# Kernel tuning notes

Hardware: AMD Instinct MI355X
Metric: run time of the kernel (lower is better)

Reference implementation:

```python
import jax, jax.numpy as jnp
import numpy as np

B, L, DIM = 8, 512, 8          # batch, seq len, raw channels (value dim D = 2*DIM = 16)
ET, HID, H = 128, 128, 2       # embed_time, hidden_size, num_heads
MAXLEN = 512
NEG = -1e9


def setup_inputs() -> dict:
    key = jax.random.key(0)
    ks = jax.random.split(key, 40)
    def n(i, shape, s=0.05):
        return jax.random.normal(ks[i], shape, jnp.float32) * s
    vals = jax.random.normal(ks[0], (B, L, DIM), jnp.float32)
    msk = (jax.random.uniform(ks[1], (B, L, DIM)) > 0.2).astype(jnp.float32)
    x = jnp.concatenate([vals, msk], -1)                      # (B, L, 2*DIM)
    time_steps = jax.random.uniform(ks[2], (B, L), jnp.float32)
    return {
        'x': x, 'time_steps': time_steps,
        # learned time embedding: Linear(1, ET-1) periodic + Linear(1,1)
        'w_per': n(3, (1, ET - 1)), 'b_per': n(4, (ET - 1,)),
        'w_lin': n(5, (1, 1)), 'b_lin': n(6, (1,)),
        # MultiTimeAttention projections
        'Wq_t': n(7, (ET, ET)), 'bq_t': n(8, (ET,)),
        'Wk_t': n(9, (ET, ET)), 'bk_t': n(10, (ET,)),
        'Wo_t': n(11, (2 * DIM * H, HID)), 'bo_t': n(12, (HID,)),
        'pos_emb': n(13, (MAXLEN + 1, HID)), 'cls_emb': n(14, (1, HID)),
        # transformer block (BERT-style post-LN encoder layer, d_ff=HID)
        'tWq': n(15, (HID, HID)), 'tbq': n(16, (HID,)),
        'tWk': n(17, (HID, HID)), 'tbk': n(18, (HID,)),
        'tWv': n(19, (HID, HID)), 'tbv': n(20, (HID,)),
        'tWo': n(21, (HID, HID)), 'tbo': n(22, (HID,)),
        'ln1_g': jnp.ones((HID,), jnp.float32), 'ln1_b': jnp.zeros((HID,), jnp.float32),
        'fW1': n(23, (HID, HID)), 'fb1': n(24, (HID,)),
        'fW2': n(25, (HID, HID)), 'fb2': n(26, (HID,)),
        'ln2_g': jnp.ones((HID,), jnp.float32), 'ln2_b': jnp.zeros((HID,), jnp.float32),
        # BertPooler
        'pW': n(27, (HID, HID)), 'pb': n(28, (HID,)),
    }


def _time_emb(tt, w_per, b_per, w_lin, b_lin):
    tt = tt[..., None]                                        # (B, L, 1)
    return jnp.concatenate([tt @ w_lin + b_lin, jnp.sin(tt @ w_per + b_per)], -1)


def _ln(x, g, b, eps=1e-5):
    m = x.mean(-1, keepdims=True)
    v = ((x - m) ** 2).mean(-1, keepdims=True)
    return (x - m) / jnp.sqrt(v + eps) * g + b


def _mta(q_emb, k_emb, value, mask, Wq, bq, Wk, bk, Wo, bo):
    # MultiTimeAttention: scores broadcast to value-channel axis, softmax over keys
    D = value.shape[-1]
    dk = ET // H
    def split(e, W, b):
        p = e @ W + b
        return p.reshape(e.shape[0], -1, H, dk).transpose(0, 2, 1, 3)
    q = split(q_emb, Wq, bq)                                  # (Bq, H, Lq, dk)
    k = split(k_emb, Wk, bk)                                  # (B,  H, Lk, dk)
    scores = jnp.matmul(q, k.swapaxes(-1, -2)) / jnp.sqrt(jnp.float32(dk))  # (B,H,Lq,Lk)
    s5 = jnp.where(mask[:, None, None, :, :] == 0, NEG, scores[..., None])  # (B,H,Lq,Lk,D)
    p = jax.nn.softmax(s5, axis=-2)
    out = jnp.einsum('bhqkd,bkd->bhqd', p, value)             # (B, H, Lq, D)
    Bv = value.shape[0]
    out = out.transpose(0, 2, 1, 3).reshape(Bv, -1, H * D)
    return out @ Wo + bo


def _tblock(x, tWq, tbq, tWk, tbk, tWv, tbv, tWo, tbo, ln1_g, ln1_b,
            fW1, fb1, fW2, fb2, ln2_g, ln2_b):
    Bq, Lq, _ = x.shape
    dk = HID // H
    def heads(W, b):
        return (x @ W + b).reshape(Bq, Lq, H, dk).transpose(0, 2, 1, 3)
    q, k, v = heads(tWq, tbq), heads(tWk, tbk), heads(tWv, tbv)
    a = jax.nn.softmax(jnp.matmul(q, k.swapaxes(-1, -2)) / jnp.sqrt(jnp.float32(dk)), -1)
    o = jnp.matmul(a, v).transpose(0, 2, 1, 3).reshape(Bq, Lq, HID) @ tWo + tbo
    x = _ln(x + o, ln1_g, ln1_b)
    f = jax.nn.relu(x @ fW1 + fb1) @ fW2 + fb2
    return _ln(x + f, ln2_g, ln2_b)


def reference(x, time_steps, w_per, b_per, w_lin, b_lin,
              Wq_t, bq_t, Wk_t, bk_t, Wo_t, bo_t, pos_emb, cls_emb,
              tWq, tbq, tWk, tbk, tWv, tbv, tWo, tbo, ln1_g, ln1_b,
              fW1, fb1, fW2, fb2, ln2_g, ln2_b, pW, pb):
    Bx = x.shape[0]
    mask_half = x[:, :, DIM:]
    mask = jnp.concatenate([mask_half, mask_half], -1)        # (B, L, 2*DIM)
    key_e = _time_emb(time_steps, w_per, b_per, w_lin, b_lin)
    tq_e = _time_emb(time_steps, w_per, b_per, w_lin, b_lin)  # query_time_steps=None -> same
    cls_t = jnp.linspace(0.0, 1.0, 128, dtype=jnp.float32)[None]
    cls_q_e = _time_emb(cls_t, w_per, b_per, w_lin, b_lin)    # (1, 128, ET)
    cls_out = _mta(cls_q_e, key_e, x, mask, Wq_t, bq_t, Wk_t, bk_t, Wo_t, bo_t)
    out = _mta(tq_e, key_e, x, mask, Wq_t, bq_t, Wk_t, bk_t, Wo_t, bo_t)
    tb = (tWq, tbq, tWk, tbk, tWv, tbv, tWo, tbo, ln1_g, ln1_b,
          fW1, fb1, fW2, fb2, ln2_g, ln2_b)
    cls_repr = jnp.broadcast_to(cls_emb[None, :, :], (Bx, 1, HID))
    # encode(cls_out, is_pooling=True), pooling='bert': no pos emb, take token 0
    h = _tblock(jnp.concatenate([cls_repr, cls_out], 1), *tb)
    cls_pooling = jnp.tanh(h[:, 0] @ pW + pb)                 # (B, HID)
    # encode(out, is_pooling=False) [pretrain path]: pos emb + transformer, drop CLS
    h2 = jnp.concatenate([cls_repr, out], 1)                  # (B, L+1, HID)
    h2 = h2 + pos_emb[:h2.shape[1]][None]
    h2 = _tblock(h2, *tb)
    last_hidden_state = h2[:, 1:]                             # (B, L, HID)
    return cls_pooling, last_hidden_state
```

## Files before the change

### kernel.cpp

```cpp
#include <hip/hip_runtime.h>
#include <hip/hip_bf16.h>
#include <math.h>


static constexpr int NM_ = 8 * 513;
static constexpr int NC_ = 8 * 129;
static constexpr int NT_ = NM_ + NC_;
static constexpr int VTS_ = 5248;

using bf = __hip_bfloat16;
typedef __attribute__((ext_vector_type(8))) short bf16x8;
typedef __attribute__((ext_vector_type(4))) short bf16x4;
typedef __attribute__((ext_vector_type(4))) float floatx4;
typedef __attribute__((ext_vector_type(8))) unsigned short ushortx8;

__device__ __forceinline__ float wave_reduce_sum(float v) {
    #pragma unroll
    for (int off = 32; off >= 1; off >>= 1) v += __shfl_xor(v, off);
    return v;
}
__device__ __forceinline__ float wave_reduce_max(float v) {
    #pragma unroll
    for (int off = 32; off >= 1; off >>= 1) v = fmaxf(v, __shfl_xor(v, off));
    return v;
// ... 76 lines not shown
        if (idx < 128 * 14) {
            int n = idx / 14, c8 = idx - n * 14;
            ushortx8 z = {0, 0, 0, 0, 0, 0, 0, 0};
            *(ushortx8*)(a.vt + (size_t)n * VTS_ + 5136 + c8 * 8) = z;
        }
    }
}

struct GemmM {
    const void* A[3]; const unsigned short* W[3]; const float* bias[3];
    unsigned short* C[3];
    int M[3]; float bscale[3];
};
__global__ void __launch_bounds__(256)
gemm_mfma_kernel(GemmM p) {
    int y = blockIdx.y;
    const unsigned short* Wsw = p.W[y];
    const float* bias = p.bias[y];
    unsigned short* C = p.C[y];
    int M = p.M[y];
    float bscale = p.bscale[y];
    int m0 = blockIdx.x * 16;
    if (m0 >= M) return;
    int tid = threadIdx.x;
    int wv = tid >> 6, lane = tid & 63;
    int am = lane & 15, aq = lane >> 4;
    const unsigned short* A = (const unsigned short*)p.A[y];
    const unsigned short* Arow = A + (size_t)(m0 + am) * 128;
    floatx4 acc0 = {0.f, 0.f, 0.f, 0.f}, acc1 = acc0;
    #pragma unroll
    for (int ks = 0; ks < 4; ++ks) {
        bf16x8 af = *(const bf16x8*)(Arow + ks * 32 + aq * 8);
        const unsigned short* base = Wsw + ((size_t)ks * 8 + 2 * wv) * 512 + lane * 8;
        bf16x8 b0 = *(const bf16x8*)(base);
        bf16x8 b1 = *(const bf16x8*)(base + 512);
        acc0 = __builtin_amdgcn_mfma_f32_16x16x32_bf16(af, b0, acc0, 0, 0, 0);
        acc1 = __builtin_amdgcn_mfma_f32_16x16x32_bf16(af, b1, acc1, 0, 0, 0);
    }
    int col = lane & 15, rowb = (lane >> 4) * 4;
    #pragma unroll
    for (int t = 0; t < 2; ++t) {
        floatx4 acc = t ? acc1 : acc0;
        int n = wv * 32 + t * 16 + col;
        float bv = bias[n] * bscale;
        #pragma unroll
        for (int rg = 0; rg < 4; ++rg)
            C[(size_t)(m0 + rowb + rg) * 128 + n] = f2u(acc[rg] + bv);
    }
}

struct MaAtt { unsigned short sp[2][16][520]; float red[2][1280]; };
union MaU { MaAtt att; unsigned short qAs[16][136]; };

__global__ void __launch_bounds__(256, 2)
mta_fused_kernel(const unsigned short* qp_cls, const unsigned short* qp_main,
                 const unsigned short* kp, const unsigned short* btg,
                 const float* Wo, const float* bo, const float* cls_emb, const float* pos,
                 float* xin,
                 const unsigned short* Wq, const unsigned short* Wk, const unsigned short* Wv,
                 const float* bq, const float* bk, const float* bv_,
                 unsigned short* outq, unsigned short* outk, unsigned short* vT) {
    __shared__ MaU U;
    __shared__ float As32[16][36];
    int vb = blockIdx.x, tid = threadIdx.x;
    int lane = tid & 63, wv = tid >> 6;
    int m = lane & 15, g = lane >> 4;
    bool special = (vb == 320);
    int is_cls = 0, qt = 0, b = 0;
    if (!special) {
        if (vb < 256) { b = vb >> 5; qt = vb & 31; }
        else { int t = vb - 256; b = t >> 3; qt = t & 7; is_cls = 1; }
    }
    int q0 = qt * 16;

    if (!special) {
        const unsigned short* qrow = is_cls
            ? (qp_cls + (size_t)(q0 + m) * 128)
            : (qp_main + (size_t)(b * 512 + q0 + m) * 128);
        bf16x8 qf[2][2];
        #pragma unroll
        for (int h = 0; h < 2; ++h) {
            qf[h][0] = *(const bf16x8*)(qrow + h * 64 + g * 8);
            qf[h][1] = *(const bf16x8*)(qrow + h * 64 + 32 + g * 8);
        }
        const unsigned short* kbase = kp + ((size_t)b * 512) * 128;
        #pragma unroll
        for (int kt = 0; kt < 8; ++kt) {
            int colk = kt * 64 + wv * 16 + m;
            const unsigned short* kb = kbase + (size_t)colk * 128;
            #pragma unroll
            for (int h = 0; h < 2; ++h) {
                bf16x8 b0 = *(const bf16x8*)(kb + h * 64 + g * 8);
                bf16x8 b1 = *(const bf16x8*)(kb + h * 64 + 32 + g * 8);
                floatx4 acc = {0.f, 0.f, 0.f, 0.f};
                acc = __builtin_amdgcn_mfma_f32_16x16x32_bf16(qf[h][0], b0, acc, 0, 0, 0);
                acc = __builtin_amdgcn_mfma_f32_16x16x32_bf16(qf[h][1], b1, acc, 0, 0, 0);
                #pragma unroll
                for (int rg = 0; rg < 4; ++rg)
                    U.att.sp[h][g * 4 + rg][colk] = f2u(acc[rg]);
            }
        }
        __syncthreads();

        for (int rr2 = wv; rr2 < 32; rr2 += 4) {
            int h = rr2 >> 4, rr = rr2 & 15;
            float mx = -1e30f;
            #pragma unroll
            for (int k = 0; k < 8; ++k) mx = fmaxf(mx, u2f(U.att.sp[h][rr][k * 64 + lane]));
            mx = wave_reduce_max(mx);
            #pragma unroll
            for (int k = 0; k < 8; ++k)
                U.att.sp[h][rr][k * 64 + lane] = f2u(expf(u2f(U.att.sp[h][rr][k * 64 + lane]) - mx));
        }
        __syncthreads();

        floatx4 macc[2] = {{0.f,0.f,0.f,0.f},{0.f,0.f,0.f,0.f}};
        {
            const unsigned short* bbase = btg + ((size_t)(b * 16 + m)) * 512 + g * 8;
            #pragma unroll
            for (int cc = 0; cc < 4; ++cc) {
                int koff = (wv + cc * 4) * 32;
                bf16x8 bfv = *(const bf16x8*)(bbase + koff);
                #pragma unroll
                for (int h = 0; h < 2; ++h) {
                    bf16x8 af = *(const bf16x8*)&U.att.sp[h][m][koff + g * 8];
                    macc[h] = __builtin_amdgcn_mfma_f32_16x16x32_bf16(af, bfv, macc[h], 0, 0, 0);
                }
            }
        }
        #pragma unroll
        for (int h = 0; h < 2; ++h)
            #pragma unroll
            for (int rg = 0; rg < 4; ++rg)
                U.att.red[h][tid * 4 + rg] = macc[h][rg];
        __syncthreads();
        {
            int l = tid >> 2, rg = tid & 3;
            int row = (l >> 4) * 4 + rg, c = l & 15;
            #pragma unroll
            for (int h = 0; h < 2; ++h) {
                const float* rc = U.att.red[h];
                float s = rc[l * 4 + rg] + rc[(64 + l) * 4 + rg]
                        + rc[(128 + l) * 4 + rg] + rc[(192 + l) * 4 + rg];
                U.att.red[h][1024 + row * 16 + c] = s;
            }
        }
        __syncthreads();
        if (tid < 128) {
            int r = tid >> 3, c = tid & 7;
            #pragma unroll
            for (int h = 0; h < 2; ++h) {
                float num = U.att.red[h][1024 + r * 16 + c];
                float den = U.att.red[h][1024 + r * 16 + 8 + c];
                As32[r][h * 16 + c] = num / den;
                As32[r][h * 16 + 8 + c] = 1.0f;
            }
        }
        __syncthreads();
    }

    int r = tid >> 4, gi = tid & 15, c0 = gi * 8;
    int segbase = is_cls ? (NM_ + b * 129) : (b * 513);
    auto Rof = [&](int rr) -> int {
        if (special) return (rr < 8) ? rr * 513 : NM_ + (rr - 8) * 129;
        return segbase + 1 + q0 + rr;
    };
    int R = Rof(r);
    int prow;
    if (special) prow = (r < 8) ? 0 : -1;
    else prow = is_cls ? -1 : (1 + q0 + r);

    float acc[8];
    if (special) {
        #pragma unroll
        for (int j = 0; j < 8; ++j) acc[j] = cls_emb[c0 + j];
    } else {
        #pragma unroll
        for (int j = 0; j < 8; ++j) acc[j] = bo[c0 + j];
        #pragma unroll 8
        for (int k = 0; k < 32; ++k) {
            float a = As32[r][k];
            const float4 w0 = *(const float4*)(Wo + (size_t)k * 128 + c0);
            const float4 w1 = *(const float4*)(Wo + (size_t)k * 128 + c0 + 4);
            acc[0] = fmaf(a, w0.x, acc[0]); acc[1] = fmaf(a, w0.y, acc[1]);
            acc[2] = fmaf(a, w0.z, acc[2]); acc[3] = fmaf(a, w0.w, acc[3]);
            acc[4] = fmaf(a, w1.x, acc[4]); acc[5] = fmaf(a, w1.y, acc[5]);
            acc[6] = fmaf(a, w1.z, acc[6]); acc[7] = fmaf(a, w1.w, acc[7]);
        }
    }
    if (prow >= 0) {
        const float* pr = pos + (size_t)prow * 128 + c0;
        float4 p0 = *(const float4*)(pr);
        float4 p1 = *(const float4*)(pr + 4);
        acc[0] += p0.x; acc[1] += p0.y; acc[2] += p0.z; acc[3] += p0.w;
        acc[4] += p1.x; acc[5] += p1.y; acc[6] += p1.z; acc[7] += p1.w;
    }
    __syncthreads();
    *(float4*)(xin + (size_t)R * 128 + c0) = make_float4(acc[0], acc[1], acc[2], acc[3]);
    *(float4*)(xin + (size_t)R * 128 + c0 + 4) = make_float4(acc[4], acc[5], acc[6], acc[7]);
    *(ushort4*)&U.qAs[r][c0] = make_ushort4(f2u(acc[0]), f2u(acc[1]), f2u(acc[2]), f2u(acc[3]));
    *(ushort4*)&U.qAs[r][c0 + 4] = make_ushort4(f2u(acc[4]), f2u(acc[5]), f2u(acc[6]), f2u(acc[7]));
    __syncthreads();

    int am = lane & 15, aq = lane >> 4;
    int col = lane & 15, rowb = (lane >> 4) * 4;
    const unsigned short* Ws[3] = {Wq, Wk, Wv};
    const float* bs[3] = {bq, bk, bv_};
    float bsc[3] = {0.125f, 1.f, 1.f};
    unsigned short* Cs[2] = {outq, outk};
    #pragma unroll
    for (int y = 0; y < 3; ++y) {
        floatx4 acc0 = {0.f, 0.f, 0.f, 0.f}, acc1 = acc0;
        #pragma unroll
        for (int ks = 0; ks < 4; ++ks) {
            bf16x8 af = *(bf16x8*)&U.qAs[am][ks * 32 + aq * 8];
            const unsigned short* base = Ws[y] + ((size_t)ks * 8 + 2 * wv) * 512 + lane * 8;
            bf16x8 b0 = *(const bf16x8*)(base);
            bf16x8 b1 = *(const bf16x8*)(base + 512);
            acc0 = __builtin_amdgcn_mfma_f32_16x16x32_bf16(af, b0, acc0, 0, 0, 0);
            acc1 = __builtin_amdgcn_mfma_f32_16x16x32_bf16(af, b1, acc1, 0, 0, 0);
        }
        #pragma unroll
        for (int t = 0; t < 2; ++t) {
            floatx4 a2 = t ? acc1 : acc0;
            int n = wv * 32 + t * 16 + col;
            float bvv = bs[y][n] * bsc[y];
            #pragma unroll
            for (int rg = 0; rg < 4; ++rg) {
                unsigned short val = f2u(a2[rg] + bvv);
                int R2 = Rof(rowb + rg);
                if (y < 2) Cs[y][(size_t)R2 * 128 + n] = val;
                else       vT[(size_t)n * VTS_ + R2] = val;
            }
        }
    }
}

union TbU {
    unsigned short sp[2][16][588];
    struct { float Xs[16][128]; unsigned short Hs[16][136]; } ffn;
};

template<int NKT>
__device__ __forceinline__ void tb_attn_phase(
    const unsigned short* qp, const unsigned short* kp, const unsigned short* vT,
    int Lq, int base, int q0, int tid,
    unsigned short (&sp)[2][16][588], float (&rinv)[2][16],
    unsigned short (&As)[16][136])
{
    int lane = tid & 63, wv = tid >> 6;
    int m = lane & 15, g = lane >> 4;

    int qr = q0 + m; if (qr >= Lq) qr = Lq - 1;
    const unsigned short* qrow = qp + (size_t)(base + qr) * 128;
    bf16x8 qf[2][2];
    #pragma unroll
    for (int h = 0; h < 2; ++h) {
        qf[h][0] = *(const bf16x8*)(qrow + h * 64 + g * 8);
        qf[h][1] = *(const bf16x8*)(qrow + h * 64 + 32 + g * 8);
    }

    #pragma unroll
    for (int kt = 0; kt < NKT; ++kt) {
        int colk = kt * 64 + wv * 16 + m;
        int krow = (colk < Lq) ? colk : (Lq - 1);
        const unsigned short* kb = kp + (size_t)(base + krow) * 128;
        #pragma unroll
        for (int h = 0; h < 2; ++h) {
            bf16x8 b0 = *(const bf16x8*)(kb + h * 64 + g * 8);
            bf16x8 b1 = *(const bf16x8*)(kb + h * 64 + 32 + g * 8);
            floatx4 acc = {0.f, 0.f, 0.f, 0.f};
            acc = __builtin_amdgcn_mfma_f32_16x16x32_bf16(qf[h][0], b0, acc, 0, 0, 0);
            acc = __builtin_amdgcn_mfma_f32_16x16x32_bf16(qf[h][1], b1, acc, 0, 0, 0);
            #pragma unroll
            for (int rg = 0; rg < 4; ++rg)
                sp[h][g * 4 + rg][colk] = f2u((colk < Lq) ? acc[rg] : -1e30f);
        }
    }
    __syncthreads();

    for (int rr2 = wv; rr2 < 32; rr2 += 4) {
        int h = rr2 >> 4, rr = rr2 & 15;
        float mx = -1e30f;
        #pragma unroll
        for (int k = 0; k < NKT; ++k) mx = fmaxf(mx, u2f(sp[h][rr][k * 64 + lane]));
        mx = wave_reduce_max(mx);
        float sum = 0.f;
        #pragma unroll
        for (int k = 0; k < NKT; ++k) {
            float e = expf(u2f(sp[h][rr][k * 64 + lane]) - mx);
            sp[h][rr][k * 64 + lane] = f2u(e);
            sum += e;
        }
        sum = wave_reduce_sum(sum);
        if (lane == 0) rinv[h][rr] = 1.f / sum;
    }
    __syncthreads();

    floatx4 oacc[2] = {{0.f,0.f,0.f,0.f},{0.f,0.f,0.f,0.f}};
    #pragma unroll
    for (int kt = 0; kt < NKT; ++kt) {
        int k0 = kt * 64;
        #pragma unroll
        for (int h = 0; h < 2; ++h) {
            const unsigned short* vbase = vT + (size_t)(h * 64 + wv * 16 + m) * VTS_ + base;
            #pragma unroll
            for (int c = 0; c < 2; ++c) {
                bf16x4 plo = *(const bf16x4*)&sp[h][m][k0 + c * 32 + g * 8];
                bf16x4 phi = *(const bf16x4*)&sp[h][m][k0 + c * 32 + g * 8 + 4];
                bf16x8 vf = *(const bf16x8*)(vbase + k0 + c * 32 + g * 8);
                oacc[h] = __builtin_amdgcn_mfma_f32_16x16x32_bf16(join8(plo, phi), vf, oacc[h], 0, 0, 0);
            }
        }
    }
    int dcol = wv * 16 + m;
    #pragma unroll
    for (int h = 0; h < 2; ++h)
        #pragma unroll
        for (int rg = 0; rg < 4; ++rg) {
            int q = g * 4 + rg;
            As[q][h * 64 + dcol] = f2u(oacc[h][rg] * rinv[h][q]);
        }
    __syncthreads();
}

__global__ void __launch_bounds__(256, 2)
tb_fused_kernel(const unsigned short* qp, const unsigned short* kp,
                const unsigned short* vT, const float* resid,
                const unsigned short* Wao, const float* bao,
                const float* g1, const float* b1ln,
                const unsigned short* W1, const float* fb1,
                const unsigned short* W2, const float* fb2,
                const float* g2, const float* b2ln,
                const float* pW, const float* pb, float* dout) {
    __shared__ TbU U;
    __shared__ unsigned short As[16][136];
    __shared__ float rinv[2][16];
    __shared__ float redS[4][4][4], redQ[4][4][4], smean[16], sinv[16], x2row[128];
    __shared__ int poolb;

    int xx = blockIdx.x, b = blockIdx.y, tid = threadIdx.x;
    int is_cls = (xx >= 33);
    int qt = is_cls ? xx - 33 : xx;
    int Lq = is_cls ? 129 : 513;
    int base = is_cls ? (NM_ + b * 129) : (b * 513);
    int lane = tid & 63, wv = tid >> 6;
    int q0 = qt * 16, g = lane >> 4;
    if (tid == 0) poolb = -1;

    if (is_cls) tb_attn_phase<3>(qp, kp, vT, Lq, base, q0, tid, U.sp, rinv, As);
    else        tb_attn_phase<9>(qp, kp, vT, Lq, base, q0, tid, U.sp, rinv, As);

    int am = lane & 15, aq = lane >> 4;
    int col = lane & 15, rowb = g * 4;

    float ov[2][4];
    {
        floatx4 acc0 = {0.f, 0.f, 0.f, 0.f}, acc1 = acc0;
        #pragma unroll
        for (int ks = 0; ks < 4; ++ks) {
            bf16x8 af = *(bf16x8*)&As[am][ks * 32 + aq * 8];
            const unsigned short* wb = Wao + ((size_t)ks * 8 + 2 * wv) * 512 + lane * 8;
            bf16x8 bb0 = *(const bf16x8*)(wb);
            bf16x8 bb1 = *(const bf16x8*)(wb + 512);
            acc0 = __builtin_amdgcn_mfma_f32_16x16x32_bf16(af, bb0, acc0, 0, 0, 0);
            acc1 = __builtin_amdgcn_mfma_f32_16x16x32_bf16(af, bb1, acc1, 0, 0, 0);
        }
        #pragma unroll
        for (int t = 0; t < 2; ++t) {
            int n = wv * 32 + t * 16 + col;
            float bv = bao[n];
            floatx4 acc = t ? acc1 : acc0;
            #pragma unroll
            for (int rg = 0; rg < 4; ++rg) {
                int qo = q0 + rowb + rg;
                int rc = (qo < Lq) ? qo : (Lq - 1);
                ov[t][rg] = acc[rg] + bv + resid[(size_t)(base + rc) * 128 + n];
            }
        }
    }
    #pragma unroll
    for (int rg = 0; rg < 4; ++rg) {
        float s = ov[0][rg] + ov[1][rg];
        float q = ov[0][rg] * ov[0][rg] + ov[1][rg] * ov[1][rg];
        #pragma unroll
        for (int off = 8; off >= 1; off >>= 1) {
            s += __shfl_xor(s, off);
            q += __shfl_xor(q, off);
        }
        if ((lane & 15) == 0) { redS[wv][g][rg] = s; redQ[wv][g][rg] = q; }
    }
    __syncthreads();
    if (tid < 16) {
        int gg = tid >> 2, rg = tid & 3;
        float s = redS[0][gg][rg] + redS[1][gg][rg] + redS[2][gg][rg] + redS[3][gg][rg];
        float q = redQ[0][gg][rg] + redQ[1][gg][rg] + redQ[2][gg][rg] + redQ[3][gg][rg];
        float mean = s * 0.0078125f;
        float var = q * 0.0078125f - mean * mean;
        smean[tid] = mean;
        sinv[tid] = rsqrtf(var + 1e-5f);
    }
    __syncthreads();
    #pragma unroll
    for (int t = 0; t < 2; ++t) {
        int n = wv * 32 + t * 16 + col;
        float gm = g1[n], bb = b1ln[n];
        #pragma unroll
        for (int rg = 0; rg < 4; ++rg) {
            int row = rowb + rg;
            float val = (ov[t][rg] - smean[row]) * sinv[row] * gm + bb;
            U.ffn.Xs[row][n] = val;
            As[row][n] = f2u(val);
        }
    }
    __syncthreads();

    {
        floatx4 acc0 = {0.f, 0.f, 0.f, 0.f}, acc1 = acc0;
        #pragma unroll
        for (int ks = 0; ks < 4; ++ks) {
            bf16x8 af = *(bf16x8*)&As[am][ks * 32 + aq * 8];
            const unsigned short* wb = W1 + ((size_t)ks * 8 + 2 * wv) * 512 + lane * 8;
            bf16x8 bb0 = *(const bf16x8*)(wb);
            bf16x8 bb1 = *(const bf16x8*)(wb + 512);
            acc0 = __builtin_amdgcn_mfma_f32_16x16x32_bf16(af, bb0, acc0, 0, 0, 0);
            acc1 = __builtin_amdgcn_mfma_f32_16x16x32_bf16(af, bb1, acc1, 0, 0, 0);
        }
        #pragma unroll
        for (int t = 0; t < 2; ++t) {
            int n = wv * 32 + t * 16 + col;
            float bv = fb1[n];
            floatx4 acc = t ? acc1 : acc0;
            #pragma unroll
            for (int rg = 0; rg < 4; ++rg)
                U.ffn.Hs[rowb + rg][n] = f2u(fmaxf(acc[rg] + bv, 0.f));
        }
    }
    __syncthreads();

    floatx4 acc0 = {0.f, 0.f, 0.f, 0.f}, acc1 = acc0;
    #pragma unroll
    for (int ks = 0; ks < 4; ++ks) {
        bf16x8 af = *(bf16x8*)&U.ffn.Hs[am][ks * 32 + aq * 8];
        const unsigned short* wb = W2 + ((size_t)ks * 8 + 2 * wv) * 512 + lane * 8;
        bf16x8 bb0 = *(const bf16x8*)(wb);
        bf16x8 bb1 = *(const bf16x8*)(wb + 512);
        acc0 = __builtin_amdgcn_mfma_f32_16x16x32_bf16(af, bb0, acc0, 0, 0, 0);
        acc1 = __builtin_amdgcn_mfma_f32_16x16x32_bf16(af, bb1, acc1, 0, 0, 0);
    }
    #pragma unroll
    for (int t = 0; t < 2; ++t) {
        int n = wv * 32 + t * 16 + col;
        float bv = fb2[n];
        floatx4 acc = t ? acc1 : acc0;
        #pragma unroll
        for (int rg = 0; rg < 4; ++rg)
            ov[t][rg] = acc[rg] + bv + U.ffn.Xs[rowb + rg][n];
    }
    #pragma unroll
    for (int rg = 0; rg < 4; ++rg) {
        float s = ov[0][rg] + ov[1][rg];
        float q = ov[0][rg] * ov[0][rg] + ov[1][rg] * ov[1][rg];
        #pragma unroll
        for (int off = 8; off >= 1; off >>= 1) {
            s += __shfl_xor(s, off);
            q += __shfl_xor(q, off);
        }
        if ((lane & 15) == 0) { redS[wv][g][rg] = s; redQ[wv][g][rg] = q; }
    }
    __syncthreads();
    if (tid < 16) {
        int gg = tid >> 2, rg = tid & 3;
        float s = redS[0][gg][rg] + redS[1][gg][rg] + redS[2][gg][rg] + redS[3][gg][rg];
        float q = redQ[0][gg][rg] + redQ[1][gg][rg] + redQ[2][gg][rg] + redQ[3][gg][rg];
        float mean = s * 0.0078125f;
        float var = q * 0.0078125f - mean * mean;
        smean[tid] = mean;
        sinv[tid] = rsqrtf(var + 1e-5f);
    }
    __syncthreads();
    #pragma unroll
    for (int t = 0; t < 2; ++t) {
        int n = wv * 32 + t * 16 + col;
        float gm = g2[n], bb = b2ln[n];
        #pragma unroll
        for (int rg = 0; rg < 4; ++rg) {
            int row = rowb + rg;
            int qout = q0 + row;
            float val = (ov[t][rg] - smean[row]) * sinv[row] * gm + bb;
            if (!is_cls) {
                if (qout >= 1 && qout < Lq)
                    dout[1024 + (size_t)b * 65536 + (size_t)(qout - 1) * 128 + n] = val;
            } else {
                if (qout == 0) {
                    x2row[n] = val;
                    if (n == 0) poolb = b;
                }
            }
        }
    }
    __syncthreads();
    if (poolb >= 0 && tid < 128) {
        float acc = pb[tid];
        for (int k = 0; k < 128; ++k) acc = fmaf(x2row[k], pW[(size_t)k * 128 + tid], acc);
        dout[(size_t)poolb * 128 + tid] = tanhf(acc);
    }
}

extern "C" void kernel_launch(void* const* d_in, const int* in_sizes, int n_in,
                              void* d_out, int out_size, void* d_ws, size_t ws_size,
                              hipStream_t stream) {
    float* w = (float*)d_ws;
    size_t off = 0;
    auto alloc = [&](size_t n) {
        float* p = w + off;
        off += (n + 3) & ~(size_t)3;
        return p;
    };
    auto allocU = [&](size_t n) { return (unsigned short*)alloc((n + 1) / 2); };

    PrepAll pa{};
    int nn = n_in < 32 ? n_in : 32;
    float* fin[32];
    const int needconv[32] = {0,0,0,0,0,0, 0,1, 0,1, 1,1, 1,1, 0,1, 0,1, 0,1,
                              0,1, 1,1, 0,1, 0,1, 1,1, 1,1};
    int ncv = 0;
    for (int i = 0; i < nn; ++i) {
        pa.src[i] = d_in[i];
        pa.n[i] = in_sizes[i];
        fin[i] = alloc(in_sizes[i]);
        pa.dstoff[i] = (int)(fin[i] - w);
        if (needconv[i]) {
            int nb = (in_sizes[i] + 255) / 256;
            pa.cstart[i] = ncv;
            pa.cnum[i] = nb;
            ncv += nb;
        } else { pa.cstart[i] = -1; pa.cnum[i] = 0; }
    }
    for (int i = nn; i < 32; ++i) {
        pa.src[i] = nullptr; pa.n[i] = 0; pa.dstoff[i] = 0;
        pa.cstart[i] = -1; pa.cnum[i] = 0;
    }
// ... 5 lines not shown
    const float* pos_emb = fin[12]; const float* cls_emb = fin[13];
    const float* tbq = fin[15]; const float* tbk = fin[17]; const float* tbv = fin[19];
    const float* tbo = fin[21];
    const float* ln1_g = fin[22]; const float* ln1_b = fin[23];
    const float* fb1 = fin[25]; const float* fb2 = fin[27];
    const float* ln2_g = fin[28]; const float* ln2_b = fin[29];
    const float* pW = fin[30]; const float* pb = fin[31];

    const int widx[8] = {8, 6, 14, 16, 18, 20, 24, 26};
    unsigned short* wsw[8];
    for (int i = 0; i < 8; ++i) {
        wsw[i] = allocU(16384);
        pa.wsrc[i] = d_in[widx[i]];
        pa.wdst[i] = wsw[i];
        pa.wscale[i] = (i == 1 || i == 2) ? 0.125f : 1.0f;
    }
    pa.ts = d_in[1]; pa.w_per = d_in[2]; pa.b_per = d_in[3];
    pa.w_lin = d_in[4]; pa.b_lin = d_in[5];
    pa.xsrc = d_in[0];
    pa.det = (const unsigned short*)d_in[22];

    unsigned short* key_e16 = allocU(4224 * 128);
    unsigned short* cls_e16 = key_e16 + 4096 * 128;
    pa.key_e16 = key_e16;
    unsigned short* btg = allocU(8 * 16 * 512);
    pa.btg = btg;

    unsigned short* qp_main16 = allocU(4096 * 128);
    unsigned short* kp_main16 = allocU(4096 * 128);
    unsigned short* qp_cls16  = allocU(128 * 128);
    float* xin     = alloc((size_t)NT_ * 128);
    unsigned short* tbq16 = allocU((size_t)NT_ * 128);
    unsigned short* tbk16 = allocU((size_t)NT_ * 128);
    unsigned short* vT    = allocU((size_t)128 * VTS_);
    pa.vt = vT;
    (void)ws_size;

    float* outf = (float*)d_out;
    int prep_nblk = ncv + 512 + 2112 + 32 + 7;

    prep_all_kernel<<<prep_nblk, 256, 0, stream>>>(pa, w);

    {
        GemmM p{};
        p.A[0] = key_e16; p.W[0] = wsw[0]; p.bias[0] = bk_t; p.C[0] = kp_main16;
        p.M[0] = 4096; p.bscale[0] = 1.f;
        p.A[1] = key_e16; p.W[1] = wsw[1]; p.bias[1] = bq_t; p.C[1] = qp_main16;
        p.M[1] = 4096; p.bscale[1] = 0.125f;
        p.A[2] = cls_e16; p.W[2] = wsw[1]; p.bias[2] = bq_t; p.C[2] = qp_cls16;
        p.M[2] = 128; p.bscale[2] = 0.125f;
        gemm_mfma_kernel<<<dim3(256, 3), 256, 0, stream>>>(p);
    }

    mta_fused_kernel<<<321, 256, 0, stream>>>(qp_cls16, qp_main16, kp_main16, btg,
                                              Wo_t, bo_t, cls_emb, pos_emb, xin,
                                              wsw[2], wsw[3], wsw[4], tbq, tbk, tbv,
                                              tbq16, tbk16, vT);

    tb_fused_kernel<<<dim3(42, 8), 256, 0, stream>>>(tbq16, tbk16, vT, xin,
                                                     wsw[5], tbo, ln1_g, ln1_b,
                                                     wsw[6], fb1, wsw[7], fb2,
                                                     ln2_g, ln2_b, pW, pb, outf);
}
```

Baseline: 203.9 us.

## Double block size to 512 threads, split heads across waves, prefetch weights

```diff
diff --git a/kernel.cpp b/kernel.cpp
--- a/kernel.cpp
+++ b/kernel.cpp
@@ -152,7 +152,7 @@
 struct MaAtt { unsigned short sp[2][16][520]; float red[2][1280]; };
 union MaU { MaAtt att; unsigned short qAs[16][136]; };
 
-__global__ void __launch_bounds__(256, 2)
+__global__ void __launch_bounds__(512, 2)
 mta_fused_kernel(const unsigned short* qp_cls, const unsigned short* qp_main,
                  const unsigned short* kp, const unsigned short* btg,
                  const float* Wo, const float* bo, const float* cls_emb, const float* pos,
@@ -163,7 +163,8 @@
     __shared__ MaU U;
     __shared__ float As32[16][36];
     int vb = blockIdx.x, tid = threadIdx.x;
-    int lane = tid & 63, wv = tid >> 6;
+    int lane = tid & 63, w = tid >> 6;
+    int h = w >> 2, ws = w & 3;
     int m = lane & 15, g = lane >> 4;
     bool special = (vb == 320);
     int is_cls = 0, qt = 0, b = 0;
@@ -174,27 +175,36 @@
     int q0 = qt * 16;
 
     if (!special) {
-        const unsigned short* qrow = is_cls
+        const unsigned short* qrow = (is_cls
             ? (qp_cls + (size_t)(q0 + m) * 128)
-            : (qp_main + (size_t)(b * 512 + q0 + m) * 128);
-        bf16x8 qf[2][2];
-        #pragma unroll
-        for (int h = 0; h < 2; ++h) {
-            qf[h][0] = *(const bf16x8*)(qrow + h * 64 + g * 8);
-            qf[h][1] = *(const bf16x8*)(qrow + h * 64 + 32 + g * 8);
-        }
-        const unsigned short* kbase = kp + ((size_t)b * 512) * 128;
-        #pragma unroll
-        for (int kt = 0; kt < 8; ++kt) {
-            int colk = kt * 64 + wv * 16 + m;
-            const unsigned short* kb = kbase + (size_t)colk * 128;
-            #pragma unroll
-            for (int h = 0; h < 2; ++h) {
-                bf16x8 b0 = *(const bf16x8*)(kb + h * 64 + g * 8);
-                bf16x8 b1 = *(const bf16x8*)(kb + h * 64 + 32 + g * 8);
+            : (qp_main + (size_t)(b * 512 + q0 + m) * 128)) + h * 64;
+        bf16x8 qf0 = *(const bf16x8*)(qrow + g * 8);
+        bf16x8 qf1 = *(const bf16x8*)(qrow + 32 + g * 8);
+        bf16x8 btf[4];
+        {
+            const unsigned short* bbase = btg + ((size_t)(b * 16 + m)) * 512 + g * 8;
+            #pragma unroll
+            for (int cc = 0; cc < 4; ++cc)
+                btf[cc] = *(const bf16x8*)(bbase + (ws + cc * 4) * 32);
+        }
+
+        const unsigned short* kbase = kp + ((size_t)b * 512) * 128 + h * 64;
+        #pragma unroll
+        for (int grp = 0; grp < 8; grp += 4) {
+            bf16x8 kf[4][2];
+            #pragma unroll
+            for (int gi = 0; gi < 4; ++gi) {
+                int colk = (grp + gi) * 64 + ws * 16 + m;
+                const unsigned short* kb = kbase + (size_t)colk * 128;
+                kf[gi][0] = *(const bf16x8*)(kb + g * 8);
+                kf[gi][1] = *(const bf16x8*)(kb + 32 + g * 8);
+            }
+            #pragma unroll
+            for (int gi = 0; gi < 4; ++gi) {
+                int colk = (grp + gi) * 64 + ws * 16 + m;
                 floatx4 acc = {0.f, 0.f, 0.f, 0.f};
-                acc = __builtin_amdgcn_mfma_f32_16x16x32_bf16(qf[h][0], b0, acc, 0, 0, 0);
-                acc = __builtin_amdgcn_mfma_f32_16x16x32_bf16(qf[h][1], b1, acc, 0, 0, 0);
+                acc = __builtin_amdgcn_mfma_f32_16x16x32_bf16(qf0, kf[gi][0], acc, 0, 0, 0);
+                acc = __builtin_amdgcn_mfma_f32_16x16x32_bf16(qf1, kf[gi][1], acc, 0, 0, 0);
                 #pragma unroll
                 for (int rg = 0; rg < 4; ++rg)
                     U.att.sp[h][g * 4 + rg][colk] = f2u(acc[rg]);
@@ -202,136 +212,129 @@
         }
         __syncthreads();
 
-        for (int rr2 = wv; rr2 < 32; rr2 += 4) {
-            int h = rr2 >> 4, rr = rr2 & 15;
+        for (int rr2 = w; rr2 < 32; rr2 += 8) {
+            int hh = rr2 >> 4, rr = rr2 & 15;
             float mx = -1e30f;
             #pragma unroll
-            for (int k = 0; k < 8; ++k) mx = fmaxf(mx, u2f(U.att.sp[h][rr][k * 64 + lane]));
+            for (int k = 0; k < 8; ++k) mx = fmaxf(mx, u2f(U.att.sp[hh][rr][k * 64 + lane]));
             mx = wave_reduce_max(mx);
             #pragma unroll
             for (int k = 0; k < 8; ++k)
-                U.att.sp[h][rr][k * 64 + lane] = f2u(expf(u2f(U.att.sp[h][rr][k * 64 + lane]) - mx));
+                U.att.sp[hh][rr][k * 64 + lane] = f2u(expf(u2f(U.att.sp[hh][rr][k * 64 + lane]) - mx));
         }
         __syncthreads();
 
-        floatx4 macc[2] = {{0.f,0.f,0.f,0.f},{0.f,0.f,0.f,0.f}};
-        {
-            const unsigned short* bbase = btg + ((size_t)(b * 16 + m)) * 512 + g * 8;
-            #pragma unroll
-            for (int cc = 0; cc < 4; ++cc) {
-                int koff = (wv + cc * 4) * 32;
-                bf16x8 bfv = *(const bf16x8*)(bbase + koff);
-                #pragma unroll
-                for (int h = 0; h < 2; ++h) {
-                    bf16x8 af = *(const bf16x8*)&U.att.sp[h][m][koff + g * 8];
-                    macc[h] = __builtin_amdgcn_mfma_f32_16x16x32_bf16(af, bfv, macc[h], 0, 0, 0);
-                }
-            }
-        }
-        #pragma unroll
-        for (int h = 0; h < 2; ++h)
-            #pragma unroll
-            for (int rg = 0; rg < 4; ++rg)
-                U.att.red[h][tid * 4 + rg] = macc[h][rg];
+        floatx4 macc = {0.f, 0.f, 0.f, 0.f};
+        #pragma unroll
+        for (int cc = 0; cc < 4; ++cc) {
+            int koff = (ws + cc * 4) * 32;
+            bf16x8 af = *(const bf16x8*)&U.att.sp[h][m][koff + g * 8];
+            macc = __builtin_amdgcn_mfma_f32_16x16x32_bf16(af, btf[cc], macc, 0, 0, 0);
+        }
+        #pragma unroll
+        for (int rg = 0; rg < 4; ++rg)
+            U.att.red[h][(ws * 64 + lane) * 4 + rg] = macc[rg];
         __syncthreads();
         {
-            int l = tid >> 2, rg = tid & 3;
+            int hh = tid >> 8, l2 = tid & 255;
+            int l = l2 >> 2, rg = l2 & 3;
+            const float* rc = U.att.red[hh];
+            float s = rc[l * 4 + rg] + rc[(64 + l) * 4 + rg]
+                    + rc[(128 + l) * 4 + rg] + rc[(192 + l) * 4 + rg];
             int row = (l >> 4) * 4 + rg, c = l & 15;
-            #pragma unroll
-            for (int h = 0; h < 2; ++h) {
-                const float* rc = U.att.red[h];
-                float s = rc[l * 4 + rg] + rc[(64 + l) * 4 + rg]
-                        + rc[(128 + l) * 4 + rg] + rc[(192 + l) * 4 + rg];
-                U.att.red[h][1024 + row * 16 + c] = s;
-            }
+            U.att.red[hh][1024 + row * 16 + c] = s;
         }
         __syncthreads();
         if (tid < 128) {
             int r = tid >> 3, c = tid & 7;
             #pragma unroll
-            for (int h = 0; h < 2; ++h) {
-                float num = U.att.red[h][1024 + r * 16 + c];
-                float den = U.att.red[h][1024 + r * 16 + 8 + c];
-                As32[r][h * 16 + c] = num / den;
-                As32[r][h * 16 + 8 + c] = 1.0f;
+            for (int hh = 0; hh < 2; ++hh) {
+                float num = U.att.red[hh][1024 + r * 16 + c];
+                float den = U.att.red[hh][1024 + r * 16 + 8 + c];
+                As32[r][hh * 16 + c] = num / den;
+                As32[r][hh * 16 + 8 + c] = 1.0f;
             }
         }
         __syncthreads();
     }
 
-    int r = tid >> 4, gi = tid & 15, c0 = gi * 8;
+    int r4 = tid >> 5, c4 = (tid & 31) * 4;
     int segbase = is_cls ? (NM_ + b * 129) : (b * 513);
     auto Rof = [&](int rr) -> int {
         if (special) return (rr < 8) ? rr * 513 : NM_ + (rr - 8) * 129;
         return segbase + 1 + q0 + rr;
     };
-    int R = Rof(r);
+    int R = Rof(r4);
     int prow;
-    if (special) prow = (r < 8) ? 0 : -1;
-    else prow = is_cls ? -1 : (1 + q0 + r);
-
-    float acc[8];
+    if (special) prow = (r4 < 8) ? 0 : -1;
+    else prow = is_cls ? -1 : (1 + q0 + r4);
+
+    float a4[4];
     if (special) {
         #pragma unroll
-        for (int j = 0; j < 8; ++j) acc[j] = cls_emb[c0 + j];
+        for (int j = 0; j < 4; ++j) a4[j] = cls_emb[c4 + j];
     } else {
         #pragma unroll
-        for (int j = 0; j < 8; ++j) acc[j] = bo[c0 + j];
-        #pragma unroll 8
-        for (int k = 0; k < 32; ++k) {
-            float a = As32[r][k];
-            const float4 w0 = *(const float4*)(Wo + (size_t)k * 128 + c0);
-            const float4 w1 = *(const float4*)(Wo + (size_t)k * 128 + c0 + 4);
-            acc[0] = fmaf(a, w0.x, acc[0]); acc[1] = fmaf(a, w0.y, acc[1]);
-            acc[2] = fmaf(a, w0.z, acc[2]); acc[3] = fmaf(a, w0.w, acc[3]);
-            acc[4] = fmaf(a, w1.x, acc[4]); acc[5] = fmaf(a, w1.y, acc[5]);
-            acc[6] = fmaf(a, w1.z, acc[6]); acc[7] = fmaf(a, w1.w, acc[7]);
+        for (int j = 0; j < 4; ++j) a4[j] = bo[c4 + j];
+        #pragma unroll
+        for (int kb0 = 0; kb0 < 32; kb0 += 8) {
+            float4 wv4[8];
+            #pragma unroll
+            for (int j = 0; j < 8; ++j)
+                wv4[j] = *(const float4*)(Wo + (size_t)(kb0 + j) * 128 + c4);
+            #pragma unroll
+            for (int j = 0; j < 8; ++j) {
+                float a = As32[r4][kb0 + j];
+                a4[0] = fmaf(a, wv4[j].x, a4[0]); a4[1] = fmaf(a, wv4[j].y, a4[1]);
+                a4[2] = fmaf(a, wv4[j].z, a4[2]); a4[3] = fmaf(a, wv4[j].w, a4[3]);
+            }
         }
     }
     if (prow >= 0) {
-        const float* pr = pos + (size_t)prow * 128 + c0;
-        float4 p0 = *(const float4*)(pr);
-        float4 p1 = *(const float4*)(pr + 4);
-        acc[0] += p0.x; acc[1] += p0.y; acc[2] += p0.z; acc[3] += p0.w;
-        acc[4] += p1.x; acc[5] += p1.y; acc[6] += p1.z; acc[7] += p1.w;
-    }
-    __syncthreads();
-    *(float4*)(xin + (size_t)R * 128 + c0) = make_float4(acc[0], acc[1], acc[2], acc[3]);
-    *(float4*)(xin + (size_t)R * 128 + c0 + 4) = make_float4(acc[4], acc[5], acc[6], acc[7]);
-    *(ushort4*)&U.qAs[r][c0] = make_ushort4(f2u(acc[0]), f2u(acc[1]), f2u(acc[2]), f2u(acc[3]));
-    *(ushort4*)&U.qAs[r][c0 + 4] = make_ushort4(f2u(acc[4]), f2u(acc[5]), f2u(acc[6]), f2u(acc[7]));
+        float4 p0 = *(const float4*)(pos + (size_t)prow * 128 + c4);
+        a4[0] += p0.x; a4[1] += p0.y; a4[2] += p0.z; a4[3] += p0.w;
+    }
+    __syncthreads();
+    *(float4*)(xin + (size_t)R * 128 + c4) = make_float4(a4[0], a4[1], a4[2], a4[3]);
+    *(ushort4*)&U.qAs[r4][c4] = make_ushort4(f2u(a4[0]), f2u(a4[1]), f2u(a4[2]), f2u(a4[3]));
     __syncthreads();
 
     int am = lane & 15, aq = lane >> 4;
     int col = lane & 15, rowb = (lane >> 4) * 4;
-    const unsigned short* Ws[3] = {Wq, Wk, Wv};
+    int n = w * 16 + col;
+    const unsigned short* Wnext[2] = {Wk, Wv};
     const float* bs[3] = {bq, bk, bv_};
     float bsc[3] = {0.125f, 1.f, 1.f};
     unsigned short* Cs[2] = {outq, outk};
+    bf16x8 wf[4];
+    #pragma unroll
+    for (int ks = 0; ks < 4; ++ks)
+        wf[ks] = *(const bf16x8*)(Wq + ((size_t)ks * 8 + w) * 512 + lane * 8);
     #pragma unroll
     for (int y = 0; y < 3; ++y) {
-        floatx4 acc0 = {0.f, 0.f, 0.f, 0.f}, acc1 = acc0;
+        bf16x8 wfn[4];
+        if (y < 2) {
+            #pragma unroll
+            for (int ks = 0; ks < 4; ++ks)
+                wfn[ks] = *(const bf16x8*)(Wnext[y] + ((size_t)ks * 8 + w) * 512 + lane * 8);
+        }
+        floatx4 acc = {0.f, 0.f, 0.f, 0.f};
         #pragma unroll
         for (int ks = 0; ks < 4; ++ks) {
             bf16x8 af = *(bf16x8*)&U.qAs[am][ks * 32 + aq * 8];
-            const unsigned short* base = Ws[y] + ((size_t)ks * 8 + 2 * wv) * 512 + lane * 8;
-            bf16x8 b0 = *(const bf16x8*)(base);
-            bf16x8 b1 = *(const bf16x8*)(base + 512);
-            acc0 = __builtin_amdgcn_mfma_f32_16x16x32_bf16(af, b0, acc0, 0, 0, 0);
-            acc1 = __builtin_amdgcn_mfma_f32_16x16x32_bf16(af, b1, acc1, 0, 0, 0);
-        }
-        #pragma unroll
-        for (int t = 0; t < 2; ++t) {
-            floatx4 a2 = t ? acc1 : acc0;
-            int n = wv * 32 + t * 16 + col;
-            float bvv = bs[y][n] * bsc[y];
-            #pragma unroll
-            for (int rg = 0; rg < 4; ++rg) {
-                unsigned short val = f2u(a2[rg] + bvv);
-                int R2 = Rof(rowb + rg);
-                if (y < 2) Cs[y][(size_t)R2 * 128 + n] = val;
-                else       vT[(size_t)n * VTS_ + R2] = val;
-            }
+            acc = __builtin_amdgcn_mfma_f32_16x16x32_bf16(af, wf[ks], acc, 0, 0, 0);
+        }
+        float bvv = bs[y][n] * bsc[y];
+        #pragma unroll
+        for (int rg = 0; rg < 4; ++rg) {
+            unsigned short val = f2u(acc[rg] + bvv);
+            int R2 = Rof(rowb + rg);
+            if (y < 2) Cs[y][(size_t)R2 * 128 + n] = val;
+            else       vT[(size_t)n * VTS_ + R2] = val;
+        }
+        if (y < 2) {
+            #pragma unroll
+            for (int ks = 0; ks < 4; ++ks) wf[ks] = wfn[ks];
         }
     }
 }
@@ -348,30 +351,32 @@
     unsigned short (&sp)[2][16][588], float (&rinv)[2][16],
     unsigned short (&As)[16][136])
 {
-    int lane = tid & 63, wv = tid >> 6;
+    int lane = tid & 63, w = tid >> 6;
+    int h = w >> 2, ws = w & 3;
     int m = lane & 15, g = lane >> 4;
 
     int qr = q0 + m; if (qr >= Lq) qr = Lq - 1;
-    const unsigned short* qrow = qp + (size_t)(base + qr) * 128;
-    bf16x8 qf[2][2];
-    #pragma unroll
-    for (int h = 0; h < 2; ++h) {
-        qf[h][0] = *(const bf16x8*)(qrow + h * 64 + g * 8);
-        qf[h][1] = *(const bf16x8*)(qrow + h * 64 + 32 + g * 8);
-    }
-
-    #pragma unroll
-    for (int kt = 0; kt < NKT; ++kt) {
-        int colk = kt * 64 + wv * 16 + m;
-        int krow = (colk < Lq) ? colk : (Lq - 1);
-        const unsigned short* kb = kp + (size_t)(base + krow) * 128;
-        #pragma unroll
-        for (int h = 0; h < 2; ++h) {
-            bf16x8 b0 = *(const bf16x8*)(kb + h * 64 + g * 8);
-            bf16x8 b1 = *(const bf16x8*)(kb + h * 64 + 32 + g * 8);
+    const unsigned short* qrow = qp + (size_t)(base + qr) * 128 + h * 64;
+    bf16x8 qf0 = *(const bf16x8*)(qrow + g * 8);
+    bf16x8 qf1 = *(const bf16x8*)(qrow + 32 + g * 8);
+
+    #pragma unroll
+    for (int grp = 0; grp < NKT; grp += 3) {
+        bf16x8 kf[3][2];
+        #pragma unroll
+        for (int gi = 0; gi < 3; ++gi) {
+            int colk = (grp + gi) * 64 + ws * 16 + m;
+            int krow = (colk < Lq) ? colk : (Lq - 1);
+            const unsigned short* kb = kp + (size_t)(base + krow) * 128 + h * 64;
+            kf[gi][0] = *(const bf16x8*)(kb + g * 8);
+            kf[gi][1] = *(const bf16x8*)(kb + 32 + g * 8);
+        }
+        #pragma unroll
+        for (int gi = 0; gi < 3; ++gi) {
+            int colk = (grp + gi) * 64 + ws * 16 + m;
             floatx4 acc = {0.f, 0.f, 0.f, 0.f};
-            acc = __builtin_amdgcn_mfma_f32_16x16x32_bf16(qf[h][0], b0, acc, 0, 0, 0);
-            acc = __builtin_amdgcn_mfma_f32_16x16x32_bf16(qf[h][1], b1, acc, 0, 0, 0);
+            acc = __builtin_amdgcn_mfma_f32_16x16x32_bf16(qf0, kf[gi][0], acc, 0, 0, 0);
+            acc = __builtin_amdgcn_mfma_f32_16x16x32_bf16(qf1, kf[gi][1], acc, 0, 0, 0);
             #pragma unroll
             for (int rg = 0; rg < 4; ++rg)
                 sp[h][g * 4 + rg][colk] = f2u((colk < Lq) ? acc[rg] : -1e30f);
@@ -379,52 +384,56 @@
     }
     __syncthreads();
 
-    for (int rr2 = wv; rr2 < 32; rr2 += 4) {
-        int h = rr2 >> 4, rr = rr2 & 15;
+    for (int rr2 = w; rr2 < 32; rr2 += 8) {
+        int hh = rr2 >> 4, rr = rr2 & 15;
         float mx = -1e30f;
         #pragma unroll
-        for (int k = 0; k < NKT; ++k) mx = fmaxf(mx, u2f(sp[h][rr][k * 64 + lane]));
+        for (int k = 0; k < NKT; ++k) mx = fmaxf(mx, u2f(sp[hh][rr][k * 64 + lane]));
         mx = wave_reduce_max(mx);
         float sum = 0.f;
         #pragma unroll
         for (int k = 0; k < NKT; ++k) {
-            float e = expf(u2f(sp[h][rr][k * 64 + lane]) - mx);
-            sp[h][rr][k * 64 + lane] = f2u(e);
+            float e = expf(u2f(sp[hh][rr][k * 64 + lane]) - mx);
+            sp[hh][rr][k * 64 + lane] = f2u(e);
             sum += e;
         }
         sum = wave_reduce_sum(sum);
-        if (lane == 0) rinv[h][rr] = 1.f / sum;
-    }
-    __syncthreads();
-
-    floatx4 oacc[2] = {{0.f,0.f,0.f,0.f},{0.f,0.f,0.f,0.f}};
-    #pragma unroll
-    for (int kt = 0; kt < NKT; ++kt) {
-        int k0 = kt * 64;
-        #pragma unroll
-        for (int h = 0; h < 2; ++h) {
-            const unsigned short* vbase = vT + (size_t)(h * 64 + wv * 16 + m) * VTS_ + base;
+        if (lane == 0) rinv[hh][rr] = 1.f / sum;
+    }
+    __syncthreads();
+
+    floatx4 oacc = {0.f, 0.f, 0.f, 0.f};
+    const unsigned short* vbase = vT + (size_t)(h * 64 + ws * 16 + m) * VTS_ + base;
+    #pragma unroll
+    for (int grp = 0; grp < NKT; grp += 3) {
+        bf16x8 vf[3][2];
+        #pragma unroll
+        for (int gi = 0; gi < 3; ++gi) {
+            int k0 = (grp + gi) * 64;
+            vf[gi][0] = *(const bf16x8*)(vbase + k0 + g * 8);
+            vf[gi][1] = *(const bf16x8*)(vbase + k0 + 32 + g * 8);
+        }
+        #pragma unroll
+        for (int gi = 0; gi < 3; ++gi) {
+            int k0 = (grp + gi) * 64;
             #pragma unroll
             for (int c = 0; c < 2; ++c) {
                 bf16x4 plo = *(const bf16x4*)&sp[h][m][k0 + c * 32 + g * 8];
                 bf16x4 phi = *(const bf16x4*)&sp[h][m][k0 + c * 32 + g * 8 + 4];
-                bf16x8 vf = *(const bf16x8*)(vbase + k0 + c * 32 + g * 8);
-                oacc[h] = __builtin_amdgcn_mfma_f32_16x16x32_bf16(join8(plo, phi), vf, oacc[h], 0, 0, 0);
+                oacc = __builtin_amdgcn_mfma_f32_16x16x32_bf16(join8(plo, phi), vf[gi][c], oacc, 0, 0, 0);
             }
         }
     }
-    int dcol = wv * 16 + m;
-    #pragma unroll
-    for (int h = 0; h < 2; ++h)
-        #pragma unroll
-        for (int rg = 0; rg < 4; ++rg) {
-            int q = g * 4 + rg;
-            As[q][h * 64 + dcol] = f2u(oacc[h][rg] * rinv[h][q]);
-        }
-    __syncthreads();
-}
-
-__global__ void __launch_bounds__(256, 2)
+    int dcol = ws * 16 + m;
+    #pragma unroll
+    for (int rg = 0; rg < 4; ++rg) {
+        int q = g * 4 + rg;
+        As[q][h * 64 + dcol] = f2u(oacc[rg] * rinv[h][q]);
+    }
+    __syncthreads();
+}
+
+__global__ void __launch_bounds__(512, 2)
 tb_fused_kernel(const unsigned short* qp, const unsigned short* kp,
                 const unsigned short* vT, const float* resid,
                 const unsigned short* Wao, const float* bao,
@@ -436,7 +445,7 @@
     __shared__ TbU U;
     __shared__ unsigned short As[16][136];
     __shared__ float rinv[2][16];
-    __shared__ float redS[4][4][4], redQ[4][4][4], smean[16], sinv[16], x2row[128];
+    __shared__ float redS[8][4][4], redQ[8][4][4], smean[16], sinv[16], x2row[128];
     __shared__ int poolb;
 
     int xx = blockIdx.x, b = blockIdx.y, tid = threadIdx.x;
@@ -444,150 +453,141 @@
     int qt = is_cls ? xx - 33 : xx;
     int Lq = is_cls ? 129 : 513;
     int base = is_cls ? (NM_ + b * 129) : (b * 513);
-    int lane = tid & 63, wv = tid >> 6;
+    int lane = tid & 63, w = tid >> 6;
     int q0 = qt * 16, g = lane >> 4;
     if (tid == 0) poolb = -1;
 
+    int am = lane & 15, aq = lane >> 4;
+    int col = lane & 15, rowb = g * 4;
+    int n = w * 16 + col;
+
+    bf16x8 waof[4];
+    #pragma unroll
+    for (int ks = 0; ks < 4; ++ks)
+        waof[ks] = *(const bf16x8*)(Wao + ((size_t)ks * 8 + w) * 512 + lane * 8);
+    float rres[4];
+    #pragma unroll
+    for (int rg = 0; rg < 4; ++rg) {
+        int qo = q0 + rowb + rg;
+        int rc = (qo < Lq) ? qo : (Lq - 1);
+        rres[rg] = resid[(size_t)(base + rc) * 128 + n];
+    }
+
     if (is_cls) tb_attn_phase<3>(qp, kp, vT, Lq, base, q0, tid, U.sp, rinv, As);
     else        tb_attn_phase<9>(qp, kp, vT, Lq, base, q0, tid, U.sp, rinv, As);
 
-    int am = lane & 15, aq = lane >> 4;
-    int col = lane & 15, rowb = g * 4;
-
-    float ov[2][4];
+    float ov[4];
+    bf16x8 w1f[4];
     {
-        floatx4 acc0 = {0.f, 0.f, 0.f, 0.f}, acc1 = acc0;
+        floatx4 acc = {0.f, 0.f, 0.f, 0.f};
         #pragma unroll
         for (int ks = 0; ks < 4; ++ks) {
             bf16x8 af = *(bf16x8*)&As[am][ks * 32 + aq * 8];
-            const unsigned short* wb = Wao + ((size_t)ks * 8 + 2 * wv) * 512 + lane * 8;
-            bf16x8 bb0 = *(const bf16x8*)(wb);
-            bf16x8 bb1 = *(const bf16x8*)(wb + 512);
-            acc0 = __builtin_amdgcn_mfma_f32_16x16x32_bf16(af, bb0, acc0, 0, 0, 0);
-            acc1 = __builtin_amdgcn_mfma_f32_16x16x32_bf16(af, bb1, acc1, 0, 0, 0);
-        }
-        #pragma unroll
-        for (int t = 0; t < 2; ++t) {
-            int n = wv * 32 + t * 16 + col;
-            float bv = bao[n];
-            floatx4 acc = t ? acc1 : acc0;
-            #pragma unroll
-            for (int rg = 0; rg < 4; ++rg) {
-                int qo = q0 + rowb + rg;
-                int rc = (qo < Lq) ? qo : (Lq - 1);
-                ov[t][rg] = acc[rg] + bv + resid[(size_t)(base + rc) * 128 + n];
-            }
-        }
+            acc = __builtin_amdgcn_mfma_f32_16x16x32_bf16(af, waof[ks], acc, 0, 0, 0);
+        }
+        #pragma unroll
+        for (int ks = 0; ks < 4; ++ks)
+            w1f[ks] = *(const bf16x8*)(W1 + ((size_t)ks * 8 + w) * 512 + lane * 8);
+        float bv = bao[n];
+        #pragma unroll
+        for (int rg = 0; rg < 4; ++rg)
+            ov[rg] = acc[rg] + bv + rres[rg];
     }
     #pragma unroll
     for (int rg = 0; rg < 4; ++rg) {
-        float s = ov[0][rg] + ov[1][rg];
-        float q = ov[0][rg] * ov[0][rg] + ov[1][rg] * ov[1][rg];
+        float s = ov[rg];
+        float q = ov[rg] * ov[rg];
         #pragma unroll
         for (int off = 8; off >= 1; off >>= 1) {
             s += __shfl_xor(s, off);
             q += __shfl_xor(q, off);
         }
-        if ((lane & 15) == 0) { redS[wv][g][rg] = s; redQ[wv][g][rg] = q; }
+        if ((lane & 15) == 0) { redS[w][g][rg] = s; redQ[w][g][rg] = q; }
     }
     __syncthreads();
     if (tid < 16) {
         int gg = tid >> 2, rg = tid & 3;
-        float s = redS[0][gg][rg] + redS[1][gg][rg] + redS[2][gg][rg] + redS[3][gg][rg];
-        float q = redQ[0][gg][rg] + redQ[1][gg][rg] + redQ[2][gg][rg] + redQ[3][gg][rg];
+        float s = 0.f, q = 0.f;
+        #pragma unroll
+        for (int ww = 0; ww < 8; ++ww) { s += redS[ww][gg][rg]; q += redQ[ww][gg][rg]; }
         float mean = s * 0.0078125f;
         float var = q * 0.0078125f - mean * mean;
         smean[tid] = mean;
         sinv[tid] = rsqrtf(var + 1e-5f);
     }
     __syncthreads();
-    #pragma unroll
-    for (int t = 0; t < 2; ++t) {
-        int n = wv * 32 + t * 16 + col;
+    {
         float gm = g1[n], bb = b1ln[n];
         #pragma unroll
         for (int rg = 0; rg < 4; ++rg) {
             int row = rowb + rg;
-            float val = (ov[t][rg] - smean[row]) * sinv[row] * gm + bb;
+            float val = (ov[rg] - smean[row]) * sinv[row] * gm + bb;
             U.ffn.Xs[row][n] = val;
             As[row][n] = f2u(val);
         }
     }
     __syncthreads();
 
+    bf16x8 w2f[4];
     {
-        floatx4 acc0 = {0.f, 0.f, 0.f, 0.f}, acc1 = acc0;
+        floatx4 acc = {0.f, 0.f, 0.f, 0.f};
         #pragma unroll
         for (int ks = 0; ks < 4; ++ks) {
             bf16x8 af = *(bf16x8*)&As[am][ks * 32 + aq * 8];
-            const unsigned short* wb = W1 + ((size_t)ks * 8 + 2 * wv) * 512 + lane * 8;
-            bf16x8 bb0 = *(const bf16x8*)(wb);
-            bf16x8 bb1 = *(const bf16x8*)(wb + 512);
-            acc0 = __builtin_amdgcn_mfma_f32_16x16x32_bf16(af, bb0, acc0, 0, 0, 0);
-            acc1 = __builtin_amdgcn_mfma_f32_16x16x32_bf16(af, bb1, acc1, 0, 0, 0);
-        }
-        #pragma unroll
-        for (int t = 0; t < 2; ++t) {
-            int n = wv * 32 + t * 16 + col;
-            float bv = fb1[n];
-            floatx4 acc = t ? acc1 : acc0;
-            #pragma unroll
-            for (int rg = 0; rg < 4; ++rg)
-                U.ffn.Hs[rowb + rg][n] = f2u(fmaxf(acc[rg] + bv, 0.f));
-        }
-    }
-    __syncthreads();
-
-    floatx4 acc0 = {0.f, 0.f, 0.f, 0.f}, acc1 = acc0;
-    #pragma unroll
-    for (int ks = 0; ks < 4; ++ks) {
-        bf16x8 af = *(bf16x8*)&U.ffn.Hs[am][ks * 32 + aq * 8];
-        const unsigned short* wb = W2 + ((size_t)ks * 8 + 2 * wv) * 512 + lane * 8;
-        bf16x8 bb0 = *(const bf16x8*)(wb);
-        bf16x8 bb1 = *(const bf16x8*)(wb + 512);
-        acc0 = __builtin_amdgcn_mfma_f32_16x16x32_bf16(af, bb0, acc0, 0, 0, 0);
-        acc1 = __builtin_amdgcn_mfma_f32_16x16x32_bf16(af, bb1, acc1, 0, 0, 0);
-    }
-    #pragma unroll
-    for (int t = 0; t < 2; ++t) {
-        int n = wv * 32 + t * 16 + col;
+            acc = __builtin_amdgcn_mfma_f32_16x16x32_bf16(af, w1f[ks], acc, 0, 0, 0);
+        }
+        #pragma unroll
+        for (int ks = 0; ks < 4; ++ks)
+            w2f[ks] = *(const bf16x8*)(W2 + ((size_t)ks * 8 + w) * 512 + lane * 8);
+        float bv = fb1[n];
+        #pragma unroll
+        for (int rg = 0; rg < 4; ++rg)
+            U.ffn.Hs[rowb + rg][n] = f2u(fmaxf(acc[rg] + bv, 0.f));
+    }
+    __syncthreads();
+
+    {
+        floatx4 acc = {0.f, 0.f, 0.f, 0.f};
+        #pragma unroll
+        for (int ks = 0; ks < 4; ++ks) {
+            bf16x8 af = *(bf16x8*)&U.ffn.Hs[am][ks * 32 + aq * 8];
+            acc = __builtin_amdgcn_mfma_f32_16x16x32_bf16(af, w2f[ks], acc, 0, 0, 0);
+        }
         float bv = fb2[n];
-        floatx4 acc = t ? acc1 : acc0;
         #pragma unroll
         for (int rg = 0; rg < 4; ++rg)
-            ov[t][rg] = acc[rg] + bv + U.ffn.Xs[rowb + rg][n];
+            ov[rg] = acc[rg] + bv + U.ffn.Xs[rowb + rg][n];
     }
     #pragma unroll
     for (int rg = 0; rg < 4; ++rg) {
-        float s = ov[0][rg] + ov[1][rg];
-        float q = ov[0][rg] * ov[0][rg] + ov[1][rg] * ov[1][rg];
+        float s = ov[rg];
+        float q = ov[rg] * ov[rg];
         #pragma unroll
         for (int off = 8; off >= 1; off >>= 1) {
             s += __shfl_xor(s, off);
             q += __shfl_xor(q, off);
         }
-        if ((lane & 15) == 0) { redS[wv][g][rg] = s; redQ[wv][g][rg] = q; }
+        if ((lane & 15) == 0) { redS[w][g][rg] = s; redQ[w][g][rg] = q; }
     }
     __syncthreads();
     if (tid < 16) {
         int gg = tid >> 2, rg = tid & 3;
-        float s = redS[0][gg][rg] + redS[1][gg][rg] + redS[2][gg][rg] + redS[3][gg][rg];
-        float q = redQ[0][gg][rg] + redQ[1][gg][rg] + redQ[2][gg][rg] + redQ[3][gg][rg];
+        float s = 0.f, q = 0.f;
+        #pragma unroll
+        for (int ww = 0; ww < 8; ++ww) { s += redS[ww][gg][rg]; q += redQ[ww][gg][rg]; }
         float mean = s * 0.0078125f;
         float var = q * 0.0078125f - mean * mean;
         smean[tid] = mean;
         sinv[tid] = rsqrtf(var + 1e-5f);
     }
     __syncthreads();
-    #pragma unroll
-    for (int t = 0; t < 2; ++t) {
-        int n = wv * 32 + t * 16 + col;
+    {
         float gm = g2[n], bb = b2ln[n];
         #pragma unroll
         for (int rg = 0; rg < 4; ++rg) {
             int row = rowb + rg;
             int qout = q0 + row;
-            float val = (ov[t][rg] - smean[row]) * sinv[row] * gm + bb;
+            float val = (ov[rg] - smean[row]) * sinv[row] * gm + bb;
             if (!is_cls) {
                 if (qout >= 1 && qout < Lq)
                     dout[1024 + (size_t)b * 65536 + (size_t)(qout - 1) * 128 + n] = val;
@@ -699,12 +699,12 @@
         gemm_mfma_kernel<<<dim3(256, 3), 256, 0, stream>>>(p);
     }
 
-    mta_fused_kernel<<<321, 256, 0, stream>>>(qp_cls16, qp_main16, kp_main16, btg,
+    mta_fused_kernel<<<321, 512, 0, stream>>>(qp_cls16, qp_main16, kp_main16, btg,
                                               Wo_t, bo_t, cls_emb, pos_emb, xin,
                                               wsw[2], wsw[3], wsw[4], tbq, tbk, tbv,
                                               tbq16, tbk16, vT);
 
-    tb_fused_kernel<<<dim3(42, 8), 256, 0, stream>>>(tbq16, tbk16, vT, xin,
+    tb_fused_kernel<<<dim3(42, 8), 512, 0, stream>>>(tbq16, tbk16, vT, xin,
                                                      wsw[5], tbo, ln1_g, ln1_b,
                                                      wsw[6], fb1, wsw[7], fb2,
                                                      ln2_g, ln2_b, pW, pb, outf);
```

New measurement: 192.7 us. -5.5%, faster.
